# Performance work log

Measured on AMD Instinct MI355X. Metric: run time of the kernel, lower is better.

Reference implementation:

```python
import jax, jax.numpy as jnp
import numpy as np

N_NODES = 50000
N_EDGES = 400000
N_GRAPHS = 64
DN = 64    # node features
DE = 64    # edge features
DG = 16    # global features
DH = 128   # mlp hidden
DO = 64    # mlp output
NHID = 2   # hidden layers
E_IN = 2 * DN + DE + DG   # 208
N_IN = DN + DO + DG       # 144


def _mlp_params(key, d_in, d_h, d_out, n_hid):
    ks = jax.random.split(key, 3)
    w_in = jax.random.normal(ks[0], (d_in, d_h), jnp.float32) * (2.0 / d_in) ** 0.5
    w_h = jax.random.normal(ks[1], (n_hid, d_h, d_h), jnp.float32) * (2.0 / d_h) ** 0.5
    w_out = jax.random.normal(ks[2], (d_h, d_out), jnp.float32) * (2.0 / d_h) ** 0.5
    return (w_in, jnp.zeros((d_h,), jnp.float32), w_h, jnp.zeros((n_hid, d_h), jnp.float32),
            w_out, jnp.zeros((d_out,), jnp.float32), jnp.ones((d_out,), jnp.float32),
            jnp.zeros((d_out,), jnp.float32))


def _mlp(h, w_in, b_in, w_h, b_h, w_out, b_out, g, b):
    # Lin -> [relu, Lin]*NHID -> relu -> Lin -> LayerNorm  (dropout=0 at eval)
    h = h @ w_in + b_in
    for i in range(w_h.shape[0]):
        h = jax.nn.relu(h) @ w_h[i] + b_h[i]
    h = jax.nn.relu(h) @ w_out + b_out
    mu = jnp.mean(h, axis=-1, keepdims=True)
    var = jnp.mean((h - mu) ** 2, axis=-1, keepdims=True)
    return (h - mu) * jax.lax.rsqrt(var + 1e-5) * g + b


def setup_inputs() -> dict:
    key = jax.random.key(0)
    k = jax.random.split(key, 8)
    x = jax.random.normal(k[0], (N_NODES, DN), jnp.float32)
    edge_attr = jax.random.normal(k[1], (N_EDGES, DE), jnp.float32)
    u = jax.random.normal(k[2], (N_GRAPHS, DG), jnp.float32)
    edge_index = jax.random.randint(k[3], (2, N_EDGES), 0, N_NODES, dtype=jnp.int32)
    batch = jnp.sort(jax.random.randint(k[4], (N_NODES,), 0, N_GRAPHS, dtype=jnp.int32))
    names = ["w_in", "b_in", "w_h", "b_h", "w_out", "b_out", "ln_g", "ln_b"]
    d = {"x": x, "edge_attr": edge_attr, "u": u, "edge_index": edge_index, "batch": batch}
    for pref, kk, d_in in (("e_", k[5], E_IN), ("a_", k[6], E_IN), ("n_", k[7], N_IN)):
        for nm, v in zip(names, _mlp_params(kk, d_in, DH, DO, NHID)):
            d[pref + nm] = v
    return d


def reference(x, edge_attr, u, edge_index, batch,
              e_w_in, e_b_in, e_w_h, e_b_h, e_w_out, e_b_out, e_ln_g, e_ln_b,
              a_w_in, a_b_in, a_w_h, a_b_h, a_w_out, a_b_out, a_ln_g, a_ln_b,
              n_w_in, n_b_in, n_w_h, n_b_h, n_w_out, n_b_out, n_ln_g, n_ln_b):
    src, tgt = edge_index[0], edge_index[1]
    edge_batch = batch[src]
    # EdgeModel: gather src/tgt node feats + global feats, concat, MLP (+ sigmoid attention MLP)
    neigh = jnp.concatenate([x[src], x[tgt], edge_attr, u[edge_batch]], axis=1)  # [E, E_IN]
    e_out = _mlp(neigh, e_w_in, e_b_in, e_w_h, e_b_h, e_w_out, e_b_out, e_ln_g, e_ln_b)
    attn = jax.nn.sigmoid(_mlp(neigh, a_w_in, a_b_in, a_w_h, a_b_h, a_w_out, a_b_out, a_ln_g, a_ln_b))
    e_out = e_out * attn  # [E, DO]
    # NodeModel: scatter-sum incoming (target-indexed) edge outputs, concat, MLP
    agg = jax.ops.segment_sum(e_out, tgt, num_segments=x.shape[0])  # [N, DO], zeros for isolated nodes
    node_in = jnp.concatenate([x, agg, u[batch]], axis=1)  # [N, N_IN]
    x_out = _mlp(node_in, n_w_in, n_b_in, n_w_h, n_b_h, n_w_out, n_b_out, n_ln_g, n_ln_b)
    return x_out
```

## Files before the change

### kernel.cpp

```cpp
#include <hip/hip_runtime.h>
#include <math.h>

#define N_NODES 50000
#define N_EDGES 400000
#define LD1 232
#define LDH 136
#define LDN 168

typedef _Float16 half8 __attribute__((ext_vector_type(8)));
typedef float f32x4 __attribute__((ext_vector_type(4)));

#define AGG_OFF 0
#define XH_OFF  12800000
#define UH_OFF  19200000
#define WP_OFF  19202048
#define O_EW1 0
#define O_EH0 28672
#define O_EH1 45056
#define O_EWO 61440
#define O_AW1 69632
#define O_AH0 98304
#define O_AH1 114688
#define O_AWO 131072
#define O_NW1 139264
#define O_NH0 159744
#define O_NH1 176128
#define O_NWO 192512

__device__ __forceinline__ f32x4 mfma16(half8 a, half8 b, f32x4 c) {
  return __builtin_amdgcn_mfma_f32_16x16x32_f16(a, b, c, 0, 0, 0);
}

__device__ __forceinline__ half8 cvt8(float4 a, float4 b) {
  half8 v;
  v[0] = (_Float16)a.x; v[1] = (_Float16)a.y; v[2] = (_Float16)a.z; v[3] = (_Float16)a.w;
  v[4] = (_Float16)b.x; v[5] = (_Float16)b.y; v[6] = (_Float16)b.z; v[7] = (_Float16)b.w;
  return v;
}

__device__ __forceinline__ half8 zero8() {
  half8 v;
#pragma unroll
  for (int j = 0; j < 8; ++j) v[j] = (_Float16)0.f;
  return v;
}

template<int NS, int LDSRC>
__device__ __forceinline__ void gemm_m2(const _Float16* __restrict__ src,
                                        _Float16* __restrict__ dst,
                                        const half8* __restrict__ wp,
                                        const float* __restrict__ bias,
                                        int w, int lane) {
  const int r = lane & 15, ch = lane >> 4;
  half8 B0[NS], B1[NS];
#pragma unroll
  for (int s = 0; s < NS; ++s) {
    B0[s] = wp[(s * 4 + ch) * 128 + w * 32 + r];
    B1[s] = wp[(s * 4 + ch) * 128 + w * 32 + 16 + r];
  }
  f32x4 a0[2], a1[2];
#pragma unroll
  for (int m = 0; m < 2; ++m) {
    a0[m] = (f32x4){0.f, 0.f, 0.f, 0.f};
    a1[m] = (f32x4){0.f, 0.f, 0.f, 0.f};
  }
#pragma unroll
  for (int s = 0; s < NS; ++s) {
#pragma unroll
    for (int m = 0; m < 2; ++m) {
      half8 a = *(const half8*)(src + (m * 16 + r) * LDSRC + s * 32 + ch * 8);
      a0[m] = mfma16(a, B0[s], a0[m]);
      a1[m] = mfma16(a, B1[s], a1[m]);
    }
  }
  float bb0 = bias[w * 32 + r], bb1 = bias[w * 32 + 16 + r];
#pragma unroll
  for (int m = 0; m < 2; ++m)
#pragma unroll
    for (int q = 0; q < 4; ++q) {
      int row = m * 16 + ch * 4 + q;
      dst[row * LDH + w * 32 + r]      = (_Float16)fmaxf(a0[m][q] + bb0, 0.f);
      dst[row * LDH + w * 32 + 16 + r] = (_Float16)fmaxf(a1[m][q] + bb1, 0.f);
    }
}

__device__ __forceinline__ void out16(const _Float16* __restrict__ src,
                                      const half8* __restrict__ wpo,
                                      const float* __restrict__ bo,
                                      const float* __restrict__ g,
                                      const float* __restrict__ bt,
                                      f32x4 acc[4], int w, int lane) {
  const int r = lane & 15, ch = lane >> 4;
  half8 BO[4][4];
#pragma unroll
  for (int s = 0; s < 4; ++s)
#pragma unroll
    for (int t = 0; t < 4; ++t) BO[s][t] = wpo[(s * 4 + ch) * 64 + t * 16 + r];
#pragma unroll
  for (int t = 0; t < 4; ++t) acc[t] = (f32x4){0.f, 0.f, 0.f, 0.f};
#pragma unroll
  for (int s = 0; s < 4; ++s) {
    half8 a = *(const half8*)(src + (w * 16 + r) * LDH + s * 32 + ch * 8);
#pragma unroll
    for (int t = 0; t < 4; ++t) acc[t] = mfma16(a, BO[s][t], acc[t]);
  }
  float g4[4], b4[4];
#pragma unroll
  for (int t = 0; t < 4; ++t) {
    float bv = bo[t * 16 + r];
#pragma unroll
    for (int q = 0; q < 4; ++q) acc[t][q] += bv;
    g4[t] = g[t * 16 + r]; b4[t] = bt[t * 16 + r];
  }
#pragma unroll
  for (int q = 0; q < 4; ++q) {
    float s1 = 0.f, s2 = 0.f;
#pragma unroll
    for (int t = 0; t < 4; ++t) { float v = acc[t][q]; s1 += v; s2 += v * v; }
#pragma unroll
    for (int mk = 1; mk < 16; mk <<= 1) {
      s1 += __shfl_xor(s1, mk); s2 += __shfl_xor(s2, mk);
    }
    float mu = s1 * (1.f / 64);
    float rs = rsqrtf(s2 * (1.f / 64) - mu * mu + 1e-5f);
#pragma unroll
    for (int t = 0; t < 4; ++t)
      acc[t][q] = (acc[t][q] - mu) * rs * g4[t] + b4[t];
  }
}

struct EdgeP {
  const float* edge_attr; const int* edge_index; const int* batch;
  const _Float16* x_h; const _Float16* u_h; const _Float16* wp;
  const float *eBin, *eBh, *eBout, *eG, *eBt;
  const float *aBin, *aBh, *aBout, *aG, *aBt;
  float* agg;
};

__global__ __launch_bounds__(256, 4) void edge_kernel(EdgeP p) {
  __shared__ __align__(16) _Float16 sIn[32 * LD1];
  __shared__ __align__(16) _Float16 sA[32 * LDH];
  __shared__ __align__(16) _Float16 sB[32 * LDH];
  const int tid = threadIdx.x, lane = tid & 63, w = tid >> 6;
  const int r = lane & 15, ch = lane >> 4;
  const int e0 = blockIdx.x * 32;

  for (int idx = tid; idx < 32 * 32; idx += 256) {
    int c = idx & 31, e = idx >> 5;
    if (c >= 28) continue;
    int col = c * 8;
    half8 v;
    if (col < 64) {
      int s = p.edge_index[e0 + e];
      v = *(const half8*)(p.x_h + (size_t)s * 64 + col);
    } else if (col < 128) {
      int t = p.edge_index[N_EDGES + e0 + e];
      v = *(const half8*)(p.x_h + (size_t)t * 64 + col - 64);
    } else if (col < 192) {
      const float* ea = p.edge_attr + (size_t)(e0 + e) * 64 + (col - 128);
      v = cvt8(*(const float4*)ea, *(const float4*)(ea + 4));
    } else if (col < 208) {
      int s = p.edge_index[e0 + e];
      int eb = p.batch[s];
      v = *(const half8*)(p.u_h + eb * 16 + col - 192);
    } else {
      v = zero8();
    }
    *(half8*)(sIn + e * LD1 + col) = v;
  }
  __syncthreads();

  gemm_m2<7, LD1>(sIn, sA, (const half8*)(p.wp + O_EW1), p.eBin, w, lane);
  __syncthreads();
  gemm_m2<4, LDH>(sA, sB, (const half8*)(p.wp + O_EH0), p.eBh, w, lane);
  __syncthreads();
  gemm_m2<4, LDH>(sB, sA, (const half8*)(p.wp + O_EH1), p.eBh + 128, w, lane);
  __syncthreads();
  half8 eP0 = zero8(), eP1 = zero8();
  if (w < 2) {
    f32x4 aE[4];
    out16(sA, (const half8*)(p.wp + O_EWO), p.eBout, p.eG, p.eBt, aE, w, lane);
#pragma unroll
    for (int q = 0; q < 4; ++q) {
      eP0[q] = (_Float16)aE[0][q]; eP0[4 + q] = (_Float16)aE[1][q];
      eP1[q] = (_Float16)aE[2][q]; eP1[4 + q] = (_Float16)aE[3][q];
    }
  }
  __syncthreads();

  gemm_m2<7, LD1>(sIn, sA, (const half8*)(p.wp + O_AW1), p.aBin, w, lane);
  __syncthreads();
  gemm_m2<4, LDH>(sA, sB, (const half8*)(p.wp + O_AH0), p.aBh, w, lane);
  __syncthreads();
  gemm_m2<4, LDH>(sB, sA, (const half8*)(p.wp + O_AH1), p.aBh + 128, w, lane);
  __syncthreads();
  if (w < 2) {
    f32x4 aA[4];
    out16(sA, (const half8*)(p.wp + O_AWO), p.aBout, p.aG, p.aBt, aA, w, lane);
    int tq[4];
#pragma unroll
    for (int q = 0; q < 4; ++q)
      tq[q] = p.edge_index[N_EDGES + e0 + w * 16 + ch * 4 + q];
#pragma unroll
    for (int q = 0; q < 4; ++q) {
      float* ap = p.agg + (size_t)tq[q] * 64 + r;
#pragma unroll
      for (int t = 0; t < 4; ++t) {
        float sg = 1.f / (1.f + __expf(-aA[t][q]));
        float oe = (t < 2) ? (float)eP0[t * 4 + q] : (float)eP1[(t - 2) * 4 + q];
        atomicAdd(ap + t * 16, oe * sg);
      }
    }
  }
}

struct NodeP {
  const float* agg; const _Float16* x_h; const _Float16* u_h;
  const _Float16* wp; const int* batch;
  const float *Bin, *Bh, *Bout, *G, *Bt;
  float* out;
};

__global__ __launch_bounds__(256, 4) void node_kernel(NodeP p) {
  __shared__ __align__(16) _Float16 sIn[32 * LDN];
  __shared__ __align__(16) _Float16 sA[32 * LDH];
  __shared__ __align__(16) _Float16 sB[32 * LDH];
  const int tid = threadIdx.x, lane = tid & 63, w = tid >> 6;
  const int r = lane & 15, ch = lane >> 4;
  const int n0 = blockIdx.x * 32;

  for (int idx = tid; idx < 32 * 32; idx += 256) {
    int c = idx & 31, e = idx >> 5;
    if (c >= 20) continue;
    int n = n0 + e, col = c * 8;
    half8 v;
    if (n >= N_NODES || col >= 144) {
      v = zero8();
    } else if (col < 64) {
      v = *(const half8*)(p.x_h + (size_t)n * 64 + col);
    } else if (col < 128) {
      const float* ag = p.agg + (size_t)n * 64 + (col - 64);
      v = cvt8(*(const float4*)ag, *(const float4*)(ag + 4));
    } else {
      v = *(const half8*)(p.u_h + p.batch[n] * 16 + col - 128);
    }
    *(half8*)(sIn + e * LDN + col) = v;
  }
  __syncthreads();

  gemm_m2<5, LDN>(sIn, sA, (const half8*)(p.wp + O_NW1), p.Bin, w, lane);
  __syncthreads();
  gemm_m2<4, LDH>(sA, sB, (const half8*)(p.wp + O_NH0), p.Bh, w, lane);
  __syncthreads();
  gemm_m2<4, LDH>(sB, sA, (const half8*)(p.wp + O_NH1), p.Bh + 128, w, lane);
  __syncthreads();
  if (w < 2) {
    f32x4 acc[4];
    out16(sA, (const half8*)(p.wp + O_NWO), p.Bout, p.G, p.Bt, acc, w, lane);
#pragma unroll
    for (int q = 0; q < 4; ++q) {
      int n = n0 + w * 16 + ch * 4 + q;
      if (n < N_NODES) {
#pragma unroll
        for (int t = 0; t < 4; ++t)
          p.out[(size_t)n * 64 + t * 16 + r] = acc[t][q];
      }
    }
  }
}

#define GX 112
struct PackP {
  const float* src[12];
  int Kreal[12], Nlog[12], size[12], dstoff[12];
  const float* x; const float* u;
  _Float16* x_h; _Float16* u_h; _Float16* wdst;
};

__global__ void pack_kernel(PackP p) {
  int y = blockIdx.y;
  int idx = blockIdx.x * 256 + threadIdx.x;
  if (y < 12) {
    int sz = p.size[y];
    if (idx >= sz) return;
    int N = 1 << p.Nlog[y];
    int j = idx & 7, t = idx >> 3;
    int n = t & (N - 1);
    int sc = t >> p.Nlog[y];
    int c = sc & 3, s = sc >> 2;
    int k = s * 32 + c * 8 + j;
    p.wdst[p.dstoff[y] + idx] =
        (k < p.Kreal[y]) ? (_Float16)p.src[y][k * N + n] : (_Float16)0.f;
  } else {
    for (int i = idx; i < N_NODES * 64; i += GX * 256) p.x_h[i] = (_Float16)p.x[i];
    for (int i = idx; i < 64 * 16; i += GX * 256) p.u_h[i] = (_Float16)p.u[i];
  }
}

extern "C" void kernel_launch(void* const* d_in, const int* in_sizes, int n_in,
                              void* d_out, int out_size, void* d_ws, size_t ws_size,
                              hipStream_t stream) {
  const float* x = (const float*)d_in[0];
  const float* edge_attr = (const float*)d_in[1];
  const float* u = (const float*)d_in[2];
  const int* edge_index = (const int*)d_in[3];
  const int* batch = (const int*)d_in[4];

  char* ws = (char*)d_ws;
  float* agg = (float*)(ws + AGG_OFF);
  _Float16* x_h = (_Float16*)(ws + XH_OFF);
  _Float16* u_h = (_Float16*)(ws + UH_OFF);
  _Float16* wp = (_Float16*)(ws + WP_OFF);

  hipMemsetAsync(agg, 0, (size_t)N_NODES * 64 * sizeof(float), stream);

  PackP pk;
  const float* eWh = (const float*)d_in[7];
  const float* aWh = (const float*)d_in[15];
  const float* nWh = (const float*)d_in[23];
  const float* srcs[12] = {
      (const float*)d_in[5], eWh, eWh + 16384, (const float*)d_in[9],
      (const float*)d_in[13], aWh, aWh + 16384, (const float*)d_in[17],
      (const float*)d_in[21], nWh, nWh + 16384, (const float*)d_in[25]};
  const int kr[12] = {208, 128, 128, 128, 208, 128, 128, 128, 144, 128, 128, 128};
  const int nl[12] = {7, 7, 7, 6, 7, 7, 7, 6, 7, 7, 7, 6};
  const int sz[12] = {28672, 16384, 16384, 8192, 28672, 16384, 16384, 8192,
                      20480, 16384, 16384, 8192};
  const int off[12] = {O_EW1, O_EH0, O_EH1, O_EWO, O_AW1, O_AH0, O_AH1, O_AWO,
                       O_NW1, O_NH0, O_NH1, O_NWO};
  for (int i = 0; i < 12; ++i) {
    pk.src[i] = srcs[i]; pk.Kreal[i] = kr[i]; pk.Nlog[i] = nl[i];
    pk.size[i] = sz[i]; pk.dstoff[i] = off[i];
  }
  pk.x = x; pk.u = u; pk.x_h = x_h; pk.u_h = u_h; pk.wdst = wp;
  pack_kernel<<<dim3(GX, 13), 256, 0, stream>>>(pk);

  EdgeP ep;
  ep.edge_attr = edge_attr; ep.edge_index = edge_index; ep.batch = batch;
  ep.x_h = x_h; ep.u_h = u_h; ep.wp = wp;
  ep.eBin = (const float*)d_in[6];  ep.eBh = (const float*)d_in[8];
  ep.eBout = (const float*)d_in[10]; ep.eG = (const float*)d_in[11];
  ep.eBt = (const float*)d_in[12];
  ep.aBin = (const float*)d_in[14]; ep.aBh = (const float*)d_in[16];
  ep.aBout = (const float*)d_in[18]; ep.aG = (const float*)d_in[19];
  ep.aBt = (const float*)d_in[20];
  ep.agg = agg;
  edge_kernel<<<N_EDGES / 32, 256, 0, stream>>>(ep);

  NodeP np;
  np.agg = agg; np.x_h = x_h; np.u_h = u_h; np.wp = wp; np.batch = batch;
  np.Bin = (const float*)d_in[22]; np.Bh = (const float*)d_in[24];
  np.Bout = (const float*)d_in[26]; np.G = (const float*)d_in[27];
  np.Bt = (const float*)d_in[28];
  np.out = (float*)d_out;
  node_kernel<<<(N_NODES + 31) / 32, 256, 0, stream>>>(np);
}
```

Before: 564.6 us.

## Run edge and attention MLPs concurrently on separate wave pairs

The edge kernel now splits its four waves so that two compute the edge MLP and two compute the attention MLP at the same time, each wave producing 64 output columns. Previously all four waves ran both MLPs one after the other, and two waves sat idle during each output layer. Edge outputs are handed to the attention waves through shared memory before the atomic scatter. Weight fragments are now loaded per k-step instead of preloaded, the pack kernel converts x in vectorized groups of eight, and the node kernel's launch-bounds occupancy hint is raised. The risks are one extra shared buffer (more LDS per block, so fewer resident blocks) and more accumulator registers per wave.

```diff
diff --git a/kernel.cpp b/kernel.cpp
--- a/kernel.cpp
+++ b/kernel.cpp
@@ -46,18 +46,49 @@
 }
 
 template<int NS, int LDSRC>
+__device__ __forceinline__ void gemm64(const _Float16* __restrict__ src,
+                                       _Float16* __restrict__ dst,
+                                       const half8* __restrict__ wp,
+                                       const float* __restrict__ bias,
+                                       int col0, int lane) {
+  const int r = lane & 15, ch = lane >> 4;
+  f32x4 acc[2][4];
+#pragma unroll
+  for (int m = 0; m < 2; ++m)
+#pragma unroll
+    for (int t = 0; t < 4; ++t) acc[m][t] = (f32x4){0.f, 0.f, 0.f, 0.f};
+#pragma unroll
+  for (int s = 0; s < NS; ++s) {
+    half8 B[4];
+#pragma unroll
+    for (int t = 0; t < 4; ++t) B[t] = wp[(s * 4 + ch) * 128 + col0 + t * 16 + r];
+    half8 A0 = *(const half8*)(src + r * LDSRC + s * 32 + ch * 8);
+    half8 A1 = *(const half8*)(src + (16 + r) * LDSRC + s * 32 + ch * 8);
+#pragma unroll
+    for (int t = 0; t < 4; ++t) {
+      acc[0][t] = mfma16(A0, B[t], acc[0][t]);
+      acc[1][t] = mfma16(A1, B[t], acc[1][t]);
+    }
+  }
+#pragma unroll
+  for (int t = 0; t < 4; ++t) {
+    float bb = bias[col0 + t * 16 + r];
+#pragma unroll
+    for (int m = 0; m < 2; ++m)
+#pragma unroll
+      for (int q = 0; q < 4; ++q)
+        dst[(m * 16 + ch * 4 + q) * LDH + col0 + t * 16 + r] =
+            (_Float16)fmaxf(acc[m][t][q] + bb, 0.f);
+  }
+}
+
+template<int NS, int LDSRC>
 __device__ __forceinline__ void gemm_m2(const _Float16* __restrict__ src,
                                         _Float16* __restrict__ dst,
                                         const half8* __restrict__ wp,
                                         const float* __restrict__ bias,
                                         int w, int lane) {
   const int r = lane & 15, ch = lane >> 4;
-  half8 B0[NS], B1[NS];
-#pragma unroll
-  for (int s = 0; s < NS; ++s) {
-    B0[s] = wp[(s * 4 + ch) * 128 + w * 32 + r];
-    B1[s] = wp[(s * 4 + ch) * 128 + w * 32 + 16 + r];
-  }
   f32x4 a0[2], a1[2];
 #pragma unroll
   for (int m = 0; m < 2; ++m) {
@@ -66,11 +97,13 @@
   }
 #pragma unroll
   for (int s = 0; s < NS; ++s) {
+    half8 B0 = wp[(s * 4 + ch) * 128 + w * 32 + r];
+    half8 B1 = wp[(s * 4 + ch) * 128 + w * 32 + 16 + r];
 #pragma unroll
     for (int m = 0; m < 2; ++m) {
       half8 a = *(const half8*)(src + (m * 16 + r) * LDSRC + s * 32 + ch * 8);
-      a0[m] = mfma16(a, B0[s], a0[m]);
-      a1[m] = mfma16(a, B1[s], a1[m]);
+      a0[m] = mfma16(a, B0, a0[m]);
+      a1[m] = mfma16(a, B1, a1[m]);
     }
   }
   float bb0 = bias[w * 32 + r], bb1 = bias[w * 32 + 16 + r];
@@ -89,20 +122,16 @@
                                       const float* __restrict__ bo,
                                       const float* __restrict__ g,
                                       const float* __restrict__ bt,
-                                      f32x4 acc[4], int w, int lane) {
+                                      f32x4 acc[4], int wh, int lane) {
   const int r = lane & 15, ch = lane >> 4;
-  half8 BO[4][4];
-#pragma unroll
-  for (int s = 0; s < 4; ++s)
-#pragma unroll
-    for (int t = 0; t < 4; ++t) BO[s][t] = wpo[(s * 4 + ch) * 64 + t * 16 + r];
 #pragma unroll
   for (int t = 0; t < 4; ++t) acc[t] = (f32x4){0.f, 0.f, 0.f, 0.f};
 #pragma unroll
   for (int s = 0; s < 4; ++s) {
-    half8 a = *(const half8*)(src + (w * 16 + r) * LDH + s * 32 + ch * 8);
-#pragma unroll
-    for (int t = 0; t < 4; ++t) acc[t] = mfma16(a, BO[s][t], acc[t]);
+    half8 a = *(const half8*)(src + (wh * 16 + r) * LDH + s * 32 + ch * 8);
+#pragma unroll
+    for (int t = 0; t < 4; ++t)
+      acc[t] = mfma16(a, wpo[(s * 4 + ch) * 64 + t * 16 + r], acc[t]);
   }
   float g4[4], b4[4];
 #pragma unroll
@@ -139,8 +168,9 @@
 
 __global__ __launch_bounds__(256, 4) void edge_kernel(EdgeP p) {
   __shared__ __align__(16) _Float16 sIn[32 * LD1];
-  __shared__ __align__(16) _Float16 sA[32 * LDH];
-  __shared__ __align__(16) _Float16 sB[32 * LDH];
+  __shared__ __align__(16) _Float16 sE[32 * LDH];
+  __shared__ __align__(16) _Float16 sA2[32 * LDH];
+  __shared__ __align__(16) _Float16 sP[32 * LDH];
   const int tid = threadIdx.x, lane = tid & 63, w = tid >> 6;
   const int r = lane & 15, ch = lane >> 4;
   const int e0 = blockIdx.x * 32;
@@ -170,45 +200,51 @@
   }
   __syncthreads();
 
-  gemm_m2<7, LD1>(sIn, sA, (const half8*)(p.wp + O_EW1), p.eBin, w, lane);
-  __syncthreads();
-  gemm_m2<4, LDH>(sA, sB, (const half8*)(p.wp + O_EH0), p.eBh, w, lane);
-  __syncthreads();
-  gemm_m2<4, LDH>(sB, sA, (const half8*)(p.wp + O_EH1), p.eBh + 128, w, lane);
-  __syncthreads();
-  half8 eP0 = zero8(), eP1 = zero8();
-  if (w < 2) {
-    f32x4 aE[4];
-    out16(sA, (const half8*)(p.wp + O_EWO), p.eBout, p.eG, p.eBt, aE, w, lane);
+  const bool isE = (w < 2);
+  const int wh = isE ? w : (w - 2);
+  const int col0 = wh * 64;
+  _Float16* ping = isE ? sE : sA2;
+  _Float16* pong = isE ? sIn : sP;
+  const half8* w1 = (const half8*)(p.wp + (isE ? O_EW1 : O_AW1));
+  const half8* h0 = (const half8*)(p.wp + (isE ? O_EH0 : O_AH0));
+  const half8* h1 = (const half8*)(p.wp + (isE ? O_EH1 : O_AH1));
+  const half8* wo = (const half8*)(p.wp + (isE ? O_EWO : O_AWO));
+  const float* bin = isE ? p.eBin : p.aBin;
+  const float* bh  = isE ? p.eBh  : p.aBh;
+  const float* bo  = isE ? p.eBout: p.aBout;
+  const float* g   = isE ? p.eG   : p.aG;
+  const float* bt  = isE ? p.eBt  : p.aBt;
+
+  gemm64<7, LD1>(sIn,  ping, w1, bin,      col0, lane); __syncthreads();
+  gemm64<4, LDH>(ping, pong, h0, bh,       col0, lane); __syncthreads();
+  gemm64<4, LDH>(pong, ping, h1, bh + 128, col0, lane); __syncthreads();
+
+  f32x4 acc[4];
+  out16(ping, wo, bo, g, bt, acc, wh, lane);
+  float* eBuf = (float*)sP;
+  if (isE) {
 #pragma unroll
     for (int q = 0; q < 4; ++q) {
-      eP0[q] = (_Float16)aE[0][q]; eP0[4 + q] = (_Float16)aE[1][q];
-      eP1[q] = (_Float16)aE[2][q]; eP1[4 + q] = (_Float16)aE[3][q];
-    }
-  }
-  __syncthreads();
-
-  gemm_m2<7, LD1>(sIn, sA, (const half8*)(p.wp + O_AW1), p.aBin, w, lane);
-  __syncthreads();
-  gemm_m2<4, LDH>(sA, sB, (const half8*)(p.wp + O_AH0), p.aBh, w, lane);
-  __syncthreads();
-  gemm_m2<4, LDH>(sB, sA, (const half8*)(p.wp + O_AH1), p.aBh + 128, w, lane);
-  __syncthreads();
-  if (w < 2) {
-    f32x4 aA[4];
-    out16(sA, (const half8*)(p.wp + O_AWO), p.aBout, p.aG, p.aBt, aA, w, lane);
+      int row = wh * 16 + ch * 4 + q;
+#pragma unroll
+      for (int t = 0; t < 4; ++t) eBuf[row * 64 + t * 16 + r] = acc[t][q];
+    }
+  }
+  __syncthreads();
+
+  if (!isE) {
     int tq[4];
 #pragma unroll
     for (int q = 0; q < 4; ++q)
-      tq[q] = p.edge_index[N_EDGES + e0 + w * 16 + ch * 4 + q];
+      tq[q] = p.edge_index[N_EDGES + e0 + wh * 16 + ch * 4 + q];
 #pragma unroll
     for (int q = 0; q < 4; ++q) {
+      int row = wh * 16 + ch * 4 + q;
       float* ap = p.agg + (size_t)tq[q] * 64 + r;
 #pragma unroll
       for (int t = 0; t < 4; ++t) {
-        float sg = 1.f / (1.f + __expf(-aA[t][q]));
-        float oe = (t < 2) ? (float)eP0[t * 4 + q] : (float)eP1[(t - 2) * 4 + q];
-        atomicAdd(ap + t * 16, oe * sg);
+        float sg = 1.f / (1.f + __expf(-acc[t][q]));
+        atomicAdd(ap + t * 16, eBuf[row * 64 + t * 16 + r] * sg);
       }
     }
   }
@@ -221,7 +257,7 @@
   float* out;
 };
 
-__global__ __launch_bounds__(256, 4) void node_kernel(NodeP p) {
+__global__ __launch_bounds__(256, 5) void node_kernel(NodeP p) {
   __shared__ __align__(16) _Float16 sIn[32 * LDN];
   __shared__ __align__(16) _Float16 sA[32 * LDH];
   __shared__ __align__(16) _Float16 sB[32 * LDH];
@@ -292,8 +328,16 @@
     p.wdst[p.dstoff[y] + idx] =
         (k < p.Kreal[y]) ? (_Float16)p.src[y][k * N + n] : (_Float16)0.f;
   } else {
-    for (int i = idx; i < N_NODES * 64; i += GX * 256) p.x_h[i] = (_Float16)p.x[i];
-    for (int i = idx; i < 64 * 16; i += GX * 256) p.u_h[i] = (_Float16)p.u[i];
+    for (int i = idx; i < N_NODES * 64 / 8; i += GX * 256) {
+      const float* s = p.x + (size_t)i * 8;
+      *(half8*)(p.x_h + (size_t)i * 8) =
+          cvt8(*(const float4*)s, *(const float4*)(s + 4));
+    }
+    for (int i = idx; i < 64 * 16 / 8; i += GX * 256) {
+      const float* s = p.u + i * 8;
+      *(half8*)(p.u_h + i * 8) =
+          cvt8(*(const float4*)s, *(const float4*)(s + 4));
+    }
   }
 }
 
```

Measured after the change: 535.2 us. -5.2%, faster.

## Split edge MLPs into persistent kernels with LDS-resident weights

Applied to the files above, without the earlier changes.

Replaces the fused edge kernel, which ran both MLPs, with two persistent 512-thread kernels: one for the edge MLP and one for the attention MLP. Each block stages its first three weight matrices into LDS once and then loops over tiles. The edge-path output goes to an fp16 workspace buffer, and the attention kernel reads it back to apply the sigmoid and do the atomic scatter. The node kernel gets the same persistent LDS-weight treatment, and the x/u fp16 conversion is vectorised to 8 elements per thread. In exchange, the edge gather runs twice and there is extra global traffic for the intermediate. Occupancy also drops to one large-LDS block per CU, and only 2 of 8 waves do the output layer.

```diff
diff --git a/kernel.cpp b/kernel.cpp
--- a/kernel.cpp
+++ b/kernel.cpp
@@ -6,6 +6,8 @@
 #define LD1 232
 #define LDH 136
 #define LDN 168
+#define N_ETILE 12500
+#define N_NTILE 1563
 
 typedef _Float16 half8 __attribute__((ext_vector_type(8)));
 typedef float f32x4 __attribute__((ext_vector_type(4)));
@@ -14,6 +16,7 @@
 #define XH_OFF  12800000
 #define UH_OFF  19200000
 #define WP_OFF  19202048
+#define EW_OFF  19603456
 #define O_EW1 0
 #define O_EH0 28672
 #define O_EH1 45056
@@ -46,42 +49,29 @@
 }
 
 template<int NS, int LDSRC>
-__device__ __forceinline__ void gemm_m2(const _Float16* __restrict__ src,
-                                        _Float16* __restrict__ dst,
-                                        const half8* __restrict__ wp,
-                                        const float* __restrict__ bias,
-                                        int w, int lane) {
+__device__ __forceinline__ void gemmL(const _Float16* __restrict__ src,
+                                      _Float16* __restrict__ dst,
+                                      const half8* __restrict__ wB,
+                                      const float* __restrict__ bias,
+                                      int w, int lane) {
   const int r = lane & 15, ch = lane >> 4;
-  half8 B0[NS], B1[NS];
+  const int c0 = w * 16;
+  f32x4 acc0 = (f32x4){0.f, 0.f, 0.f, 0.f};
+  f32x4 acc1 = (f32x4){0.f, 0.f, 0.f, 0.f};
 #pragma unroll
   for (int s = 0; s < NS; ++s) {
-    B0[s] = wp[(s * 4 + ch) * 128 + w * 32 + r];
-    B1[s] = wp[(s * 4 + ch) * 128 + w * 32 + 16 + r];
-  }
-  f32x4 a0[2], a1[2];
-#pragma unroll
-  for (int m = 0; m < 2; ++m) {
-    a0[m] = (f32x4){0.f, 0.f, 0.f, 0.f};
-    a1[m] = (f32x4){0.f, 0.f, 0.f, 0.f};
-  }
-#pragma unroll
-  for (int s = 0; s < NS; ++s) {
-#pragma unroll
-    for (int m = 0; m < 2; ++m) {
-      half8 a = *(const half8*)(src + (m * 16 + r) * LDSRC + s * 32 + ch * 8);
-      a0[m] = mfma16(a, B0[s], a0[m]);
-      a1[m] = mfma16(a, B1[s], a1[m]);
-    }
-  }
-  float bb0 = bias[w * 32 + r], bb1 = bias[w * 32 + 16 + r];
-#pragma unroll
-  for (int m = 0; m < 2; ++m)
-#pragma unroll
-    for (int q = 0; q < 4; ++q) {
-      int row = m * 16 + ch * 4 + q;
-      dst[row * LDH + w * 32 + r]      = (_Float16)fmaxf(a0[m][q] + bb0, 0.f);
-      dst[row * LDH + w * 32 + 16 + r] = (_Float16)fmaxf(a1[m][q] + bb1, 0.f);
-    }
+    half8 B  = wB[(s * 4 + ch) * 128 + c0 + r];
+    half8 A0 = *(const half8*)(src + r * LDSRC + s * 32 + ch * 8);
+    half8 A1 = *(const half8*)(src + (16 + r) * LDSRC + s * 32 + ch * 8);
+    acc0 = mfma16(A0, B, acc0);
+    acc1 = mfma16(A1, B, acc1);
+  }
+  float bb = bias[c0 + r];
+#pragma unroll
+  for (int q = 0; q < 4; ++q) {
+    dst[(ch * 4 + q) * LDH + c0 + r]      = (_Float16)fmaxf(acc0[q] + bb, 0.f);
+    dst[(16 + ch * 4 + q) * LDH + c0 + r] = (_Float16)fmaxf(acc1[q] + bb, 0.f);
+  }
 }
 
 __device__ __forceinline__ void out16(const _Float16* __restrict__ src,
@@ -89,20 +79,16 @@
                                       const float* __restrict__ bo,
                                       const float* __restrict__ g,
                                       const float* __restrict__ bt,
-                                      f32x4 acc[4], int w, int lane) {
+                                      f32x4 acc[4], int wh, int lane) {
   const int r = lane & 15, ch = lane >> 4;
-  half8 BO[4][4];
-#pragma unroll
-  for (int s = 0; s < 4; ++s)
-#pragma unroll
-    for (int t = 0; t < 4; ++t) BO[s][t] = wpo[(s * 4 + ch) * 64 + t * 16 + r];
 #pragma unroll
   for (int t = 0; t < 4; ++t) acc[t] = (f32x4){0.f, 0.f, 0.f, 0.f};
 #pragma unroll
   for (int s = 0; s < 4; ++s) {
-    half8 a = *(const half8*)(src + (w * 16 + r) * LDH + s * 32 + ch * 8);
-#pragma unroll
-    for (int t = 0; t < 4; ++t) acc[t] = mfma16(a, BO[s][t], acc[t]);
+    half8 a = *(const half8*)(src + (wh * 16 + r) * LDH + s * 32 + ch * 8);
+#pragma unroll
+    for (int t = 0; t < 4; ++t)
+      acc[t] = mfma16(a, wpo[(s * 4 + ch) * 64 + t * 16 + r], acc[t]);
   }
   float g4[4], b4[4];
 #pragma unroll
@@ -129,143 +115,173 @@
   }
 }
 
-struct EdgeP {
+struct PathP {
   const float* edge_attr; const int* edge_index; const int* batch;
   const _Float16* x_h; const _Float16* u_h; const _Float16* wp;
-  const float *eBin, *eBh, *eBout, *eG, *eBt;
-  const float *aBin, *aBh, *aBout, *aG, *aBt;
+  const float *Bin, *Bh, *Bout, *G, *Bt;
+  _Float16* eW;
   float* agg;
+  int w1_off, h0_off, h1_off, wo_off;
 };
 
-__global__ __launch_bounds__(256, 4) void edge_kernel(EdgeP p) {
-  __shared__ __align__(16) _Float16 sIn[32 * LD1];
-  __shared__ __align__(16) _Float16 sA[32 * LDH];
-  __shared__ __align__(16) _Float16 sB[32 * LDH];
+template<bool IS_A>
+__global__ __launch_bounds__(512, 2) void path_kernel(PathP p) {
+  extern __shared__ char smem[];
+  half8* wL1 = (half8*)smem;
+  half8* wH0 = (half8*)(smem + 57344);
+  half8* wH1 = (half8*)(smem + 90112);
+  _Float16* sIn   = (_Float16*)(smem + 122880);
+  _Float16* sPing = (_Float16*)(smem + 137728);
+  _Float16* sPong = (_Float16*)(smem + 146432);
+
   const int tid = threadIdx.x, lane = tid & 63, w = tid >> 6;
   const int r = lane & 15, ch = lane >> 4;
-  const int e0 = blockIdx.x * 32;
-
-  for (int idx = tid; idx < 32 * 32; idx += 256) {
-    int c = idx & 31, e = idx >> 5;
-    if (c >= 28) continue;
-    int col = c * 8;
-    half8 v;
-    if (col < 64) {
-      int s = p.edge_index[e0 + e];
-      v = *(const half8*)(p.x_h + (size_t)s * 64 + col);
-    } else if (col < 128) {
-      int t = p.edge_index[N_EDGES + e0 + e];
-      v = *(const half8*)(p.x_h + (size_t)t * 64 + col - 64);
-    } else if (col < 192) {
-      const float* ea = p.edge_attr + (size_t)(e0 + e) * 64 + (col - 128);
-      v = cvt8(*(const float4*)ea, *(const float4*)(ea + 4));
-    } else if (col < 208) {
-      int s = p.edge_index[e0 + e];
-      int eb = p.batch[s];
-      v = *(const half8*)(p.u_h + eb * 16 + col - 192);
-    } else {
-      v = zero8();
-    }
-    *(half8*)(sIn + e * LD1 + col) = v;
+
+  {
+    const half8* g1 = (const half8*)(p.wp + p.w1_off);
+    const half8* g2 = (const half8*)(p.wp + p.h0_off);
+    const half8* g3 = (const half8*)(p.wp + p.h1_off);
+    for (int i = tid; i < 3584; i += 512) wL1[i] = g1[i];
+    for (int i = tid; i < 2048; i += 512) wH0[i] = g2[i];
+    for (int i = tid; i < 2048; i += 512) wH1[i] = g3[i];
   }
   __syncthreads();
 
-  gemm_m2<7, LD1>(sIn, sA, (const half8*)(p.wp + O_EW1), p.eBin, w, lane);
-  __syncthreads();
-  gemm_m2<4, LDH>(sA, sB, (const half8*)(p.wp + O_EH0), p.eBh, w, lane);
-  __syncthreads();
-  gemm_m2<4, LDH>(sB, sA, (const half8*)(p.wp + O_EH1), p.eBh + 128, w, lane);
-  __syncthreads();
-  half8 eP0 = zero8(), eP1 = zero8();
-  if (w < 2) {
-    f32x4 aE[4];
-    out16(sA, (const half8*)(p.wp + O_EWO), p.eBout, p.eG, p.eBt, aE, w, lane);
-#pragma unroll
-    for (int q = 0; q < 4; ++q) {
-      eP0[q] = (_Float16)aE[0][q]; eP0[4 + q] = (_Float16)aE[1][q];
-      eP1[q] = (_Float16)aE[2][q]; eP1[4 + q] = (_Float16)aE[3][q];
-    }
-  }
-  __syncthreads();
-
-  gemm_m2<7, LD1>(sIn, sA, (const half8*)(p.wp + O_AW1), p.aBin, w, lane);
-  __syncthreads();
-  gemm_m2<4, LDH>(sA, sB, (const half8*)(p.wp + O_AH0), p.aBh, w, lane);
-  __syncthreads();
-  gemm_m2<4, LDH>(sB, sA, (const half8*)(p.wp + O_AH1), p.aBh + 128, w, lane);
-  __syncthreads();
-  if (w < 2) {
-    f32x4 aA[4];
-    out16(sA, (const half8*)(p.wp + O_AWO), p.aBout, p.aG, p.aBt, aA, w, lane);
-    int tq[4];
-#pragma unroll
-    for (int q = 0; q < 4; ++q)
-      tq[q] = p.edge_index[N_EDGES + e0 + w * 16 + ch * 4 + q];
-#pragma unroll
-    for (int q = 0; q < 4; ++q) {
-      float* ap = p.agg + (size_t)tq[q] * 64 + r;
-#pragma unroll
-      for (int t = 0; t < 4; ++t) {
-        float sg = 1.f / (1.f + __expf(-aA[t][q]));
-        float oe = (t < 2) ? (float)eP0[t * 4 + q] : (float)eP1[(t - 2) * 4 + q];
-        atomicAdd(ap + t * 16, oe * sg);
+  const half8* wpo = (const half8*)(p.wp + p.wo_off);
+
+  for (int tile = blockIdx.x; tile < N_ETILE; tile += gridDim.x) {
+    const int e0 = tile * 32;
+
+    for (int idx = tid; idx < 1024; idx += 512) {
+      int c = idx & 31, e = idx >> 5;
+      if (c >= 28) continue;
+      int col = c * 8;
+      half8 v;
+      if (col < 64) {
+        int s = p.edge_index[e0 + e];
+        v = *(const half8*)(p.x_h + (size_t)s * 64 + col);
+      } else if (col < 128) {
+        int t = p.edge_index[N_EDGES + e0 + e];
+        v = *(const half8*)(p.x_h + (size_t)t * 64 + col - 64);
+      } else if (col < 192) {
+        const float* ea = p.edge_attr + (size_t)(e0 + e) * 64 + (col - 128);
+        v = cvt8(*(const float4*)ea, *(const float4*)(ea + 4));
+      } else if (col < 208) {
+        int s = p.edge_index[e0 + e];
+        int eb = p.batch[s];
+        v = *(const half8*)(p.u_h + eb * 16 + col - 192);
+      } else {
+        v = zero8();
       }
-    }
-  }
-}
-
-struct NodeP {
+      *(half8*)(sIn + e * LD1 + col) = v;
+    }
+    __syncthreads();
+
+    gemmL<7, LD1>(sIn, sPing, wL1, p.Bin, w, lane);        __syncthreads();
+    gemmL<4, LDH>(sPing, sPong, wH0, p.Bh, w, lane);       __syncthreads();
+    gemmL<4, LDH>(sPong, sPing, wH1, p.Bh + 128, w, lane); __syncthreads();
+
+    if (w < 2) {
+      f32x4 acc[4];
+      out16(sPing, wpo, p.Bout, p.G, p.Bt, acc, w, lane);
+      if (!IS_A) {
+#pragma unroll
+        for (int q = 0; q < 4; ++q) {
+          int row = w * 16 + ch * 4 + q;
+          _Float16* d = p.eW + (size_t)(e0 + row) * 64 + r;
+#pragma unroll
+          for (int t = 0; t < 4; ++t) d[t * 16] = (_Float16)acc[t][q];
+        }
+      } else {
+#pragma unroll
+        for (int q = 0; q < 4; ++q) {
+          int row = w * 16 + ch * 4 + q;
+          int tq = p.edge_index[N_EDGES + e0 + row];
+          const _Float16* es = p.eW + (size_t)(e0 + row) * 64 + r;
+          float* ap = p.agg + (size_t)tq * 64 + r;
+#pragma unroll
+          for (int t = 0; t < 4; ++t) {
+            float sg = 1.f / (1.f + __expf(-acc[t][q]));
+            atomicAdd(ap + t * 16, (float)es[t * 16] * sg);
+          }
+        }
+      }
+    }
+    __syncthreads();
+  }
+}
+
+struct NodePP {
   const float* agg; const _Float16* x_h; const _Float16* u_h;
   const _Float16* wp; const int* batch;
   const float *Bin, *Bh, *Bout, *G, *Bt;
   float* out;
 };
 
-__global__ __launch_bounds__(256, 4) void node_kernel(NodeP p) {
-  __shared__ __align__(16) _Float16 sIn[32 * LDN];
-  __shared__ __align__(16) _Float16 sA[32 * LDH];
-  __shared__ __align__(16) _Float16 sB[32 * LDH];
+__global__ __launch_bounds__(512, 2) void node_kernel(NodePP p) {
+  extern __shared__ char smem[];
+  half8* wL1 = (half8*)smem;
+  half8* wH0 = (half8*)(smem + 40960);
+  half8* wH1 = (half8*)(smem + 73728);
+  _Float16* sIn   = (_Float16*)(smem + 106496);
+  _Float16* sPing = (_Float16*)(smem + 117248);
+  _Float16* sPong = (_Float16*)(smem + 125952);
+
   const int tid = threadIdx.x, lane = tid & 63, w = tid >> 6;
   const int r = lane & 15, ch = lane >> 4;
-  const int n0 = blockIdx.x * 32;
-
-  for (int idx = tid; idx < 32 * 32; idx += 256) {
-    int c = idx & 31, e = idx >> 5;
-    if (c >= 20) continue;
-    int n = n0 + e, col = c * 8;
-    half8 v;
-    if (n >= N_NODES || col >= 144) {
-      v = zero8();
-    } else if (col < 64) {
-      v = *(const half8*)(p.x_h + (size_t)n * 64 + col);
-    } else if (col < 128) {
-      const float* ag = p.agg + (size_t)n * 64 + (col - 64);
-      v = cvt8(*(const float4*)ag, *(const float4*)(ag + 4));
-    } else {
-      v = *(const half8*)(p.u_h + p.batch[n] * 16 + col - 128);
-    }
-    *(half8*)(sIn + e * LDN + col) = v;
+
+  {
+    const half8* g1 = (const half8*)(p.wp + O_NW1);
+    const half8* g2 = (const half8*)(p.wp + O_NH0);
+    const half8* g3 = (const half8*)(p.wp + O_NH1);
+    for (int i = tid; i < 2560; i += 512) wL1[i] = g1[i];
+    for (int i = tid; i < 2048; i += 512) wH0[i] = g2[i];
+    for (int i = tid; i < 2048; i += 512) wH1[i] = g3[i];
   }
   __syncthreads();
 
-  gemm_m2<5, LDN>(sIn, sA, (const half8*)(p.wp + O_NW1), p.Bin, w, lane);
-  __syncthreads();
-  gemm_m2<4, LDH>(sA, sB, (const half8*)(p.wp + O_NH0), p.Bh, w, lane);
-  __syncthreads();
-  gemm_m2<4, LDH>(sB, sA, (const half8*)(p.wp + O_NH1), p.Bh + 128, w, lane);
-  __syncthreads();
-  if (w < 2) {
-    f32x4 acc[4];
-    out16(sA, (const half8*)(p.wp + O_NWO), p.Bout, p.G, p.Bt, acc, w, lane);
-#pragma unroll
-    for (int q = 0; q < 4; ++q) {
-      int n = n0 + w * 16 + ch * 4 + q;
-      if (n < N_NODES) {
-#pragma unroll
-        for (int t = 0; t < 4; ++t)
-          p.out[(size_t)n * 64 + t * 16 + r] = acc[t][q];
+  const half8* wpo = (const half8*)(p.wp + O_NWO);
+
+  for (int tile = blockIdx.x; tile < N_NTILE; tile += gridDim.x) {
+    const int n0 = tile * 32;
+
+    for (int idx = tid; idx < 1024; idx += 512) {
+      int c = idx & 31, e = idx >> 5;
+      if (c >= 20) continue;
+      int n = n0 + e, col = c * 8;
+      half8 v;
+      if (n >= N_NODES || col >= 144) {
+        v = zero8();
+      } else if (col < 64) {
+        v = *(const half8*)(p.x_h + (size_t)n * 64 + col);
+      } else if (col < 128) {
+        const float* ag = p.agg + (size_t)n * 64 + (col - 64);
+        v = cvt8(*(const float4*)ag, *(const float4*)(ag + 4));
+      } else {
+        v = *(const half8*)(p.u_h + p.batch[n] * 16 + col - 128);
       }
-    }
+      *(half8*)(sIn + e * LDN + col) = v;
+    }
+    __syncthreads();
+
+    gemmL<5, LDN>(sIn, sPing, wL1, p.Bin, w, lane);        __syncthreads();
+    gemmL<4, LDH>(sPing, sPong, wH0, p.Bh, w, lane);       __syncthreads();
+    gemmL<4, LDH>(sPong, sPing, wH1, p.Bh + 128, w, lane); __syncthreads();
+
+    if (w < 2) {
+      f32x4 acc[4];
+      out16(sPing, wpo, p.Bout, p.G, p.Bt, acc, w, lane);
+#pragma unroll
+      for (int q = 0; q < 4; ++q) {
+        int n = n0 + w * 16 + ch * 4 + q;
+        if (n < N_NODES) {
+#pragma unroll
+          for (int t = 0; t < 4; ++t)
+            p.out[(size_t)n * 64 + t * 16 + r] = acc[t][q];
+        }
+      }
+    }
+    __syncthreads();
   }
 }
 
@@ -292,8 +308,16 @@
     p.wdst[p.dstoff[y] + idx] =
         (k < p.Kreal[y]) ? (_Float16)p.src[y][k * N + n] : (_Float16)0.f;
   } else {
-    for (int i = idx; i < N_NODES * 64; i += GX * 256) p.x_h[i] = (_Float16)p.x[i];
-    for (int i = idx; i < 64 * 16; i += GX * 256) p.u_h[i] = (_Float16)p.u[i];
+    for (int i = idx; i < N_NODES * 64 / 8; i += GX * 256) {
+      const float* s = p.x + (size_t)i * 8;
+      *(half8*)(p.x_h + (size_t)i * 8) =
+          cvt8(*(const float4*)s, *(const float4*)(s + 4));
+    }
+    for (int i = idx; i < 64 * 16 / 8; i += GX * 256) {
+      const float* s = p.u + i * 8;
+      *(half8*)(p.u_h + i * 8) =
+          cvt8(*(const float4*)s, *(const float4*)(s + 4));
+    }
   }
 }
 
@@ -311,6 +335,7 @@
   _Float16* x_h = (_Float16*)(ws + XH_OFF);
   _Float16* u_h = (_Float16*)(ws + UH_OFF);
   _Float16* wp = (_Float16*)(ws + WP_OFF);
+  _Float16* eW = (_Float16*)(ws + EW_OFF);
 
   hipMemsetAsync(agg, 0, (size_t)N_NODES * 64 * sizeof(float), stream);
 
@@ -335,23 +360,28 @@
   pk.x = x; pk.u = u; pk.x_h = x_h; pk.u_h = u_h; pk.wdst = wp;
   pack_kernel<<<dim3(GX, 13), 256, 0, stream>>>(pk);
 
-  EdgeP ep;
+  PathP ep;
   ep.edge_attr = edge_attr; ep.edge_index = edge_index; ep.batch = batch;
   ep.x_h = x_h; ep.u_h = u_h; ep.wp = wp;
-  ep.eBin = (const float*)d_in[6];  ep.eBh = (const float*)d_in[8];
-  ep.eBout = (const float*)d_in[10]; ep.eG = (const float*)d_in[11];
-  ep.eBt = (const float*)d_in[12];
-  ep.aBin = (const float*)d_in[14]; ep.aBh = (const float*)d_in[16];
-  ep.aBout = (const float*)d_in[18]; ep.aG = (const float*)d_in[19];
-  ep.aBt = (const float*)d_in[20];
-  ep.agg = agg;
-  edge_kernel<<<N_EDGES / 32, 256, 0, stream>>>(ep);
-
-  NodeP np;
+  ep.eW = eW; ep.agg = agg;
+
+  ep.Bin = (const float*)d_in[6];  ep.Bh = (const float*)d_in[8];
+  ep.Bout = (const float*)d_in[10]; ep.G = (const float*)d_in[11];
+  ep.Bt = (const float*)d_in[12];
+  ep.w1_off = O_EW1; ep.h0_off = O_EH0; ep.h1_off = O_EH1; ep.wo_off = O_EWO;
+  path_kernel<false><<<512, 512, 155136, stream>>>(ep);
+
+  ep.Bin = (const float*)d_in[14]; ep.Bh = (const float*)d_in[16];
+  ep.Bout = (const float*)d_in[18]; ep.G = (const float*)d_in[19];
+  ep.Bt = (const float*)d_in[20];
+  ep.w1_off = O_AW1; ep.h0_off = O_AH0; ep.h1_off = O_AH1; ep.wo_off = O_AWO;
+  path_kernel<true><<<512, 512, 155136, stream>>>(ep);
+
+  NodePP np;
   np.agg = agg; np.x_h = x_h; np.u_h = u_h; np.wp = wp; np.batch = batch;
   np.Bin = (const float*)d_in[22]; np.Bh = (const float*)d_in[24];
   np.Bout = (const float*)d_in[26]; np.G = (const float*)d_in[27];
   np.Bt = (const float*)d_in[28];
   np.out = (float*)d_out;
-  node_kernel<<<(N_NODES + 31) / 32, 256, 0, stream>>>(np);
-}
+  node_kernel<<<512, 512, 134656, stream>>>(np);
+}
```

After: 1.320 ms. +133.8%, slower.
